# Kernel optimization log

Hardware: AMD Instinct MI355X
Metric: run time of the kernel (lower is better)

## Reference

```python
import jax, jax.numpy as jnp
import numpy as np

BS, CH, T = 128, 16, 12288
RED = 6          # mini_window_temporal_reduction_factor
N = CH * RED     # 96 mini-windows
K = 5            # top-k selected mini-windows
NCLS = 5
LATENT = (T // 16) * 8  # hypernet flatten dim = 6144


def _conv1d(x, w, b=None):
    # x: [B,C,L], w: [O,I,ks] -> [B,O,L-ks+1]
    out = jax.lax.conv_general_dilated(x, w, (1,), 'VALID', dimension_numbers=('NCH', 'OIH', 'NCH'))
    return out if b is None else out + b[None, :, None]


def _same_reflect(x, w, b):
    p = (w.shape[-1] - 1) // 2
    return _conv1d(jnp.pad(x, ((0, 0), (0, 0), (p, p)), mode='reflect'), w, b)


def _leaky(z):
    return jnp.where(z >= 0, z, 0.01 * z)


def _pool(x, f, op):
    L = x.shape[-1] // f  # floor, drop remainder (matches torch pooling)
    xr = x[..., :L * f].reshape(x.shape[:-1] + (L, f))
    return op(xr, -1)


def setup_inputs() -> dict:
    key = jax.random.key(0)
    ks = jax.random.split(key, 18)
    s = 0.05
    return {
        'x': jax.random.normal(ks[0], (BS, CH, T), jnp.float32),
        'epoch': 0,
        # hypernet conv blocks (padding='same', reflect)
        'hw1': jax.random.normal(ks[1], (32, CH, 7), jnp.float32) * s,
        'hb1': jnp.zeros((32,), jnp.float32),
        'hw2': jax.random.normal(ks[2], (64, 32, 7), jnp.float32) * s,
        'hb2': jnp.zeros((64,), jnp.float32),
        'hw3': jax.random.normal(ks[3], (8, 64, 7), jnp.float32) * s,
        'hb3': jnp.zeros((8,), jnp.float32),
        'hl1': jax.random.normal(ks[4], (N, LATENT), jnp.float32) * s,  # Linear(latent->N), no bias
        'hl2': jax.random.normal(ks[5], (N, N), jnp.float32) * s,       # Linear(N->N), no bias
        # GroupedIdxConv1D: per-group Conv1d(1, 64, ks=15); bias only for group 0
        'gw': jax.random.normal(ks[6], (CH, 64, 15), jnp.float32) * s,
        'gb0': jax.random.normal(ks[7], (64,), jnp.float32) * s,
        # encoder convs 1,2
        'ew2': jax.random.normal(ks[8], (128, 64, 7), jnp.float32) * s,
        'eb2': jnp.zeros((128,), jnp.float32),
        'ew3': jax.random.normal(ks[9], (128, 128, 7), jnp.float32) * s,
        'eb3': jnp.zeros((128,), jnp.float32),
        # classifier
        'cw': jax.random.normal(ks[10], (NCLS, 128), jnp.float32) * s,
        'cb': jnp.zeros((NCLS,), jnp.float32),
    }


def reference(x, epoch, hw1, hb1, hw2, hb2, hw3, hb3, hl1, hl2, gw, gb0, ew2, eb2, ew3, eb3, cw, cb):
    # Eval-mode forward (active sampling, no Gumbel noise, hard top-k one-hot, dropout off)
    bs = x.shape[0]
    # ---- hypernet ----
    h = _pool(_leaky(_same_reflect(x, hw1, hb1)), 4, jnp.mean)
    h = _pool(_leaky(_same_reflect(h, hw2, hb2)), 4, jnp.mean)
    h = jnp.tanh(_same_reflect(h, hw3, hb3)).reshape(bs, -1)
    logits = _leaky(h @ hl1.T) @ hl2.T  # [bs, N]
    # ---- hard top-k sampling (bmm with one-hot == gather rows) ----
    _, idx = jax.lax.top_k(logits, K)                      # [bs, K]
    x_r = x.reshape(bs, N, -1)                             # [bs, N, T']
    sel = jnp.take_along_axis(x_r, idx[:, :, None], axis=1)  # [bs, K, T']
    gidx = idx // RED                                      # ExG channel group per mini-window
    # ---- GroupedIdxConv1D: per-element kernel gather + conv + sum over K ----
    ksz = gw.shape[-1]
    Lout = sel.shape[-1] - ksz + 1
    windows = jnp.stack([sel[..., i:i + Lout] for i in range(ksz)], axis=-1)  # [bs,K,Lout,ksz]
    kernels = gw[gidx]                                     # [bs,K,64,ksz]
    z = jnp.einsum('bkls,bkos->bol', windows, kernels)     # conv + sum over channel axis K
    n0 = (gidx == 0).sum(1).astype(z.dtype)                # bias only for group 0 elements
    z = z + n0[:, None, None] * gb0[None, :, None]
    # ---- encoder tail ----
    z = _pool(_leaky(z), 4, jnp.max)
    z = _pool(_leaky(_conv1d(z, ew2, eb2)), 4, jnp.max)
    z = _conv1d(z, ew3, eb3).mean(-1)                      # AdaptiveAvgPool1d(1) -> [bs,128]
    # ---- classifier ----
    return jax.nn.log_softmax(z @ cw.T + cb, -1)           # [bs, NCLS]
```

## Files before the change

kernel.cpp:

```cpp
#include <hip/hip_runtime.h>
#include <hip/hip_bf16.h>
#include <math.h>

typedef unsigned short u16;
typedef __attribute__((ext_vector_type(8))) short short8;
typedef __attribute__((ext_vector_type(4))) float floatx4;

__device__ __forceinline__ float lk(float v){ return v >= 0.f ? v : 0.01f*v; }
__device__ __forceinline__ u16 f2b(float f){
    __hip_bfloat16 h = __float2bfloat16(f);
    return *reinterpret_cast<u16*>(&h);
}
__device__ __forceinline__ int refl(int t, int L){
    return t < 0 ? -t : (t >= L ? 2*L-2-t : t);
}

__global__ __launch_bounds__(256,6) void k_hconv1(const float* __restrict__ x,
        const float* __restrict__ w, const float* __restrict__ bias,
        u16* __restrict__ h1)
{
    __shared__ __align__(16) u16 xs[2][264*24];
    int b = blockIdx.x / 24, pb = blockIdx.x % 24;
    int tid = threadIdx.x;
    const float* xb = x + (size_t)b*16*12288;
    int wv = tid >> 6, lane = tid & 63;
    int m = lane & 15, kq = lane >> 4;
    int ohalf = wv & 1, thalf = wv >> 1;
    int o = ohalf*16 + m;

    short8 wfr[4];
    #pragma unroll
    for (int s=0;s<4;s++){
        int tap = 2*s + (kq>>1);
        #pragma unroll
        for (int j=0;j<8;j++){
            int ic = (kq&1)*8 + j;
            wfr[s][j] = (tap < 7) ? (short)f2b(w[(o*16+ic)*7 + tap]) : (short)0;
        }
    }

    float rg0[16]; float rgx;
    int exrow = 256 + (tid>>4), exch = tid & 15;

#define LOADTILE(G0) { \
        int t0 = refl((G0) - 3 + tid, 12288); \
        _Pragma("unroll") \
        for (int ic=0;ic<16;ic++) rg0[ic] = xb[(size_t)ic*12288 + t0]; \
        if (tid < 128){ \
            int t1 = refl((G0) - 3 + exrow, 12288); \
            rgx = xb[(size_t)exch*12288 + t1]; \
        } }

#define WRITETILE(BUF) { \
        short8 p0, p1; \
        _Pragma("unroll") \
        for (int j=0;j<8;j++){ p0[j] = (short)f2b(rg0[j]); p1[j] = (short)f2b(rg0[8+j]); } \
        *reinterpret_cast<short8*>(&xs[BUF][tid*24])     = p0; \
        *reinterpret_cast<short8*>(&xs[BUF][tid*24 + 8]) = p1; \
        if (tid < 128) xs[BUF][exrow*24 + exch] = f2b(rgx); }

#define COMPUTESTORE(BUF, TILE) { \
        floatx4 acc[8]; \
        _Pragma("unroll") \
        for (int i=0;i<8;i++) acc[i] = (floatx4){0.f,0.f,0.f,0.f}; \
        int tb0 = thalf*128; \
        _Pragma("unroll") \
        for (int sub=0; sub<8; sub++){ \
            int tb = tb0 + sub*16; \
            _Pragma("unroll") \
            for (int s=0;s<4;s++){ \
                int tap = 2*s + (kq>>1); \
                short8 xfr = *reinterpret_cast<const short8*>( \
                                &xs[BUF][(tb + m + tap)*24 + (kq&1)*8]); \
                acc[sub] = __builtin_amdgcn_mfma_f32_16x16x32_bf16(xfr, wfr[s], acc[sub], 0,0,0); \
            } \
        } \
        float bv = bias[o]; \
        size_t base = ((size_t)b*3072 + (TILE)*64 + thalf*32 + kq)*32 + o; \
        _Pragma("unroll") \
        for (int sub=0; sub<8; sub++){ \
            float sum = lk(acc[sub][0]+bv) + lk(acc[sub][1]+bv) \
                      + lk(acc[sub][2]+bv) + lk(acc[sub][3]+bv); \
            h1[base + (size_t)sub*128] = f2b(sum*0.25f); \
        } }

    int g0 = pb*512;
    LOADTILE(g0);
    WRITETILE(0);
    __syncthreads();
    LOADTILE(g0 + 256);
    COMPUTESTORE(0, pb*2);
    WRITETILE(1);
    __syncthreads();
    COMPUTESTORE(1, pb*2 + 1);

#undef LOADTILE
#undef WRITETILE
#undef COMPUTESTORE
}

__global__ __launch_bounds__(256,4) void k_hconv2(const u16* __restrict__ h1,
        const float* __restrict__ w, const float* __restrict__ bias,
        float* __restrict__ h2)
{
    __shared__ __align__(16) u16 xs[2][198*40];
    int b = blockIdx.x >> 3, tile = blockIdx.x & 7;
    int tid = threadIdx.x;
    int wv = tid >> 6, lane = tid & 63;
    int m = lane & 15, kq = lane >> 4;
    int o = wv*16 + m;

    short8 wfr[7];
    #pragma unroll
    for (int s=0;s<7;s++){
        #pragma unroll
        for (int j=0;j<8;j++)
            wfr[s][j] = (short)f2b(w[(size_t)(o*32 + kq*8 + j)*7 + s]);
    }

    short8 rgA[3], rgX;

#define LOADH(HALF) { \
        int gh = tile*384 + (HALF)*192 - 3; \
        _Pragma("unroll") \
        for (int cc=0;cc<3;cc++){ \
            int c = tid + cc*256; \
            int row = c >> 2, q = c & 3; \
            int t = refl(gh + row, 3072); \
            rgA[cc] = *reinterpret_cast<const short8*>(&h1[((size_t)b*3072 + t)*32 + q*8]); \
        } \
        if (tid < 24){ \
            int c = 768 + tid; \
            int row = c >> 2, q = c & 3; \
            int t = refl(gh + row, 3072); \
            rgX = *reinterpret_cast<const short8*>(&h1[((size_t)b*3072 + t)*32 + q*8]); \
        } }

#define WRITEH(BUF) { \
        _Pragma("unroll") \
        for (int cc=0;cc<3;cc++){ \
            int c = tid + cc*256; \
            *reinterpret_cast<short8*>(&xs[BUF][(c>>2)*40 + (c&3)*8]) = rgA[cc]; \
        } \
        if (tid < 24){ \
            int c = 768 + tid; \
            *reinterpret_cast<short8*>(&xs[BUF][(c>>2)*40 + (c&3)*8]) = rgX; \
        } }

#define COMPUTEH(BUF, HALF) { \
        floatx4 acc[12]; \
        _Pragma("unroll") \
        for (int i=0;i<12;i++) acc[i] = (floatx4){0.f,0.f,0.f,0.f}; \
        for (int sub=0; sub<12; sub++){ \
            int tb = sub*16; \
            _Pragma("unroll") \
            for (int s=0;s<7;s++){ \
                short8 xfr = *reinterpret_cast<const short8*>( \
                                &xs[BUF][(tb + m + s)*40 + kq*8]); \
                acc[sub] = __builtin_amdgcn_mfma_f32_16x16x32_bf16(xfr, wfr[s], acc[sub], 0,0,0); \
            } \
        } \
        float bv = bias[o]; \
        _Pragma("unroll") \
        for (int sub=0; sub<12; sub++){ \
            float sum = lk(acc[sub][0]+bv) + lk(acc[sub][1]+bv) \
                      + lk(acc[sub][2]+bv) + lk(acc[sub][3]+bv); \
            h2[((size_t)b*768 + tile*96 + (HALF)*48 + sub*4 + kq)*64 + o] = sum*0.25f; \
        } }

    LOADH(0);
    WRITEH(0);
    __syncthreads();
    LOADH(1);
    COMPUTEH(0, 0);
    WRITEH(1);
    __syncthreads();
    COMPUTEH(1, 1);

#undef LOADH
#undef WRITEH
#undef COMPUTEH
}

__global__ __launch_bounds__(256) void k_hconv3(const float* __restrict__ h2,
        const float* __restrict__ w, const float* __restrict__ bias,
        float* __restrict__ latent)
{
    __shared__ float xs[64*201];
    int b = blockIdx.x >> 2, tile = blockIdx.x & 3;
    int g0 = tile*192;
    int tid = threadIdx.x;
    for (int idx = tid; idx < 198*64; idx += 256){
        int jj = idx >> 6, ic = idx & 63;
        int t = refl(g0 + jj - 3, 768);
        xs[ic*201 + jj] = h2[((size_t)b*768 + t)*64 + ic];
    }
    __syncthreads();
    int c = tid >> 5, run = tid & 31;
    int p0 = run*6;
    float acc[6];
    #pragma unroll
    for (int l=0;l<6;l++) acc[l] = 0.f;
    for (int ic=0; ic<64; ic++){
        const float* wp = w + (c*64+ic)*7;
        float wr[7];
        #pragma unroll
        for (int s=0;s<7;s++) wr[s] = wp[s];
        const float* xr = xs + ic*201 + p0;
        float xw[12];
        #pragma unroll
        for (int j=0;j<12;j++) xw[j] = xr[j];
        #pragma unroll
        for (int s=0;s<7;s++)
            #pragma unroll
            for (int l=0;l<6;l++) acc[l] += wr[s]*xw[l+s];
    }
    float bv = bias[c];
    float* op = latent + (size_t)b*6144 + c*768 + g0 + p0;
    #pragma unroll
    for (int l=0;l<6;l++) op[l] = tanhf(acc[l] + bv);
}

__global__ __launch_bounds__(256) void k_lin1(const float* __restrict__ latent,
        const float* __restrict__ hl1, float* __restrict__ t1)
{
    __shared__ float ls[6144];
    int b = blockIdx.x / 6, ntile = blockIdx.x % 6;
    int tid = threadIdx.x;
    const float4* lp = reinterpret_cast<const float4*>(latent + (size_t)b*6144);
    float4* lsv = reinterpret_cast<float4*>(ls);
    for (int i = tid; i < 1536; i += 256) lsv[i] = lp[i];
    __syncthreads();
    int wv = tid >> 6, lane = tid & 63;
    #pragma unroll
    for (int nn=0; nn<4; nn++){
        int n = ntile*16 + wv*4 + nn;
        const float4* wp = reinterpret_cast<const float4*>(hl1 + (size_t)n*6144);
        float s = 0.f;
        #pragma unroll
        for (int j=0;j<24;j++){
            float4 q = wp[lane + 64*j];
            float4 l4 = lsv[lane + 64*j];
            s += l4.x*q.x + l4.y*q.y + l4.z*q.z + l4.w*q.w;
        }
        #pragma unroll
        for (int off=32; off; off>>=1) s += __shfl_down(s, off);
        if (lane==0) t1[b*96+n] = lk(s);
    }
}

__global__ __launch_bounds__(128) void k_topk(const float* __restrict__ t1,
        const float* __restrict__ hl2, int* __restrict__ idxb, float* __restrict__ n0f)
{
    __shared__ float lg[96];
    int b = blockIdx.x, n = threadIdx.x;
    if (n < 96){
        float s = 0.f;
        const float* tp = t1 + b*96;
        const float* wp = hl2 + n*96;
        for (int m=0;m<96;m++) s += tp[m]*wp[m];
        lg[n] = s;
    }
    __syncthreads();
    if (threadIdx.x == 0){
        unsigned long long u0=0ull, u1=0ull;
        float n0 = 0.f;
        for (int k=0;k<5;k++){
            float best = -3.4e38f; int bi = 0;
            for (int m=0;m<96;m++){
                bool used = m<64 ? ((u0>>m)&1ull) : ((u1>>(m-64))&1ull);
                if (!used && lg[m] > best){ best = lg[m]; bi = m; }
            }
            if (bi<64) u0 |= 1ull<<bi; else u1 |= 1ull<<(bi-64);
            idxb[b*5+k] = bi;
            if (bi < 6) n0 += 1.f;
        }
        n0f[b] = n0;
    }
}

__global__ __launch_bounds__(256,3) void k_gconv(const float* __restrict__ x,
        const int* __restrict__ idxb, const float* __restrict__ n0f,
        const float* __restrict__ gw, const float* __restrict__ gb0,
        u16* __restrict__ zp)
{
    __shared__ __align__(16) u16 xs[5][8][536];
    __shared__ int nidx[5];
    __shared__ float n0s;
    int b = blockIdx.x >> 2, qc = blockIdx.x & 3;
    int tid = threadIdx.x;
    int p0g = qc*512;

    if (tid < 5) nidx[tid] = idxb[b*5 + tid];
    if (tid == 5) n0s = n0f[b];
    __syncthreads();

    for (int cch = tid; cch < 5*134; cch += 256){
        int k = cch / 134, q = cch - k*134;
        const float* xrow = x + (size_t)b*196608 + (size_t)nidx[k]*2048;
        int base = p0g + q*4;
        u16 vb[4];
        if (base + 3 <= 2047){
            float4 a = *reinterpret_cast<const float4*>(xrow + base);
            vb[0]=f2b(a.x); vb[1]=f2b(a.y); vb[2]=f2b(a.z); vb[3]=f2b(a.w);
        } else {
            #pragma unroll
            for (int jj=0;jj<4;jj++){
                int ii = base+jj; if (ii > 2047) ii = 2047;
                vb[jj] = f2b(xrow[ii]);
            }
        }
        #pragma unroll
        for (int jj=0;jj<4;jj++){
            int gof = q*4 + jj;
            #pragma unroll
            for (int r=0;r<8;r++){
                int i = gof - r;
                if (i >= 0 && i < 528) xs[k][r][i] = vb[jj];
            }
        }
    }

    int wv = tid >> 6, lane = tid & 63;
    int m = lane & 15, kq = lane >> 4;
    int o = wv*16 + m;

    short8 wfr[3];
    #pragma unroll
    for (int c=0;c<3;c++){
        #pragma unroll
        for (int j=0;j<8;j++){
            int k = 32*c + kq*8 + j;
            int kk = k >> 4, tap = k & 15;
            short v = 0;
            if (kk < 5 && tap < 15){
                int gi = nidx[kk] / 6;
                v = (short)f2b(gw[(size_t)gi*960 + o*15 + tap]);
            }
            wfr[c][j] = v;
        }
    }
    float bv = n0s * gb0[o];
    __syncthreads();

    int rr = m & 7, ibase = (m & 8) + (kq & 1)*8;
    for (int g8 = 0; g8 < 4; ++g8){
        floatx4 acc[8];
        #pragma unroll
        for (int i=0;i<8;i++) acc[i] = (floatx4){0.f,0.f,0.f,0.f};
        #pragma unroll
        for (int s8=0; s8<8; ++s8){
            int P = (g8*8 + s8)*16;
            #pragma unroll
            for (int c=0;c<3;c++){
                int kk = 2*c + (kq>>1);
                int kkc = kk < 5 ? kk : 4;
                short8 af = *reinterpret_cast<const short8*>(&xs[kkc][rr][P + ibase]);
                acc[s8] = __builtin_amdgcn_mfma_f32_16x16x32_bf16(af, wfr[c], acc[s8], 0,0,0);
            }
        }
        #pragma unroll
        for (int s8=0; s8<8; ++s8){
            int sub = g8*8 + s8;
            int Q = qc*128 + sub*4 + kq;
            if (Q < 508){
                float mx = fmaxf(fmaxf(lk(acc[s8][0]+bv), lk(acc[s8][1]+bv)),
                                 fmaxf(lk(acc[s8][2]+bv), lk(acc[s8][3]+bv)));
                zp[((size_t)b*508 + Q)*64 + o] = f2b(mx);
            }
        }
    }
}

__global__ __launch_bounds__(256,1) void k_econv2(const u16* __restrict__ zp,
        const float* __restrict__ w, const float* __restrict__ bias,
        float* __restrict__ p2)
{
    __shared__ __align__(16) u16 xs[118*72];
    int b = blockIdx.x / 5, tile = blockIdx.x % 5;
    int tid = threadIdx.x;
    for (int c = tid; c < 118*8; c += 256){
        int row = c >> 3, q = c & 7;
        int t = tile*100 + row; if (t > 507) t = 507;
        *reinterpret_cast<short8*>(&xs[row*72 + q*8]) =
            *reinterpret_cast<const short8*>(&zp[((size_t)b*508 + t)*64 + q*8]);
    }
    __syncthreads();
    int wv = tid >> 6, lane = tid & 63;
    int m = lane & 15, kq = lane >> 4;
    for (int half=0; half<2; half++){
        int ot = wv + 4*half;
        int o = ot*16 + m;
        short8 wfr[14];
        #pragma unroll
        for (int s=0;s<14;s++){
            int ih = s/7, tap = s%7;
            #pragma unroll
            for (int j=0;j<8;j++)
                wfr[s][j] = (short)f2b(w[(size_t)(o*64 + ih*32 + kq*8 + j)*7 + tap]);
        }
        floatx4 acc[7];
        #pragma unroll
        for (int i=0;i<7;i++) acc[i] = (floatx4){0.f,0.f,0.f,0.f};
        #pragma unroll
        for (int sub=0; sub<7; sub++){
            #pragma unroll
            for (int s=0;s<14;s++){
                int ih = s/7, tap = s%7;
                short8 xfr = *reinterpret_cast<const short8*>(
                                &xs[(sub*16 + m + tap)*72 + ih*32 + kq*8]);
                acc[sub] = __builtin_amdgcn_mfma_f32_16x16x32_bf16(xfr, wfr[s], acc[sub], 0,0,0);
            }
        }
        float bv = bias[o];
        #pragma unroll
        for (int sub=0; sub<7; sub++){
            int pidx = sub*4 + kq;
            if (pidx < 25){
                float mx = fmaxf(fmaxf(lk(acc[sub][0]+bv), lk(acc[sub][1]+bv)),
                                 fmaxf(lk(acc[sub][2]+bv), lk(acc[sub][3]+bv)));
                p2[((size_t)b*125 + tile*25 + pidx)*128 + o] = mx;
            }
        }
    }
}

__global__ __launch_bounds__(128) void k_tail(const float* __restrict__ p2,
        const float* __restrict__ w, const float* __restrict__ bias,
        const float* __restrict__ cw, const float* __restrict__ cb,
        float* __restrict__ out)
{
    __shared__ float ss[7][128];
    __shared__ float ft[128];
    __shared__ float lgs[5];
    int b = blockIdx.x, tid = threadIdx.x;

    {
        const float* pb = p2 + (size_t)b*125*128 + tid;
        float first6[6], last6[6];
        float c = 0.f;
        #pragma unroll
        for (int t=0;t<6;t++){ float v = pb[(size_t)t*128]; first6[t]=v; c+=v; }
        for (int t=6;t<119;t++) c += pb[(size_t)t*128];
        #pragma unroll
        for (int t=0;t<6;t++) last6[t] = pb[(size_t)(119+t)*128];
        ss[0][tid] = c;
        #pragma unroll
        for (int s=0;s<6;s++){ c = c - first6[s] + last6[s]; ss[s+1][tid] = c; }
    }
    __syncthreads();

    {
        const float* wp = w + (size_t)tid*896;
        float s = 0.f;
        for (int ic=0; ic<128; ic++){
            #pragma unroll
            for (int tp=0; tp<7; tp++)
                s += wp[ic*7+tp]*ss[tp][ic];
        }
        ft[tid] = s*(1.f/119.f) + bias[tid];
    }
    __syncthreads();

    if (tid < 5){
        float lg = cb[tid];
        const float* wp = cw + tid*128;
        for (int o=0;o<128;o++) lg += ft[o]*wp[o];
        lgs[tid] = lg;
    }
    __syncthreads();
    if (tid == 0){
        float mx = -3.4e38f;
        for (int c=0;c<5;c++) mx = fmaxf(mx, lgs[c]);
        float se = 0.f;
        for (int c=0;c<5;c++) se += expf(lgs[c]-mx);
        float lse = mx + logf(se);
        for (int c=0;c<5;c++) out[b*5+c] = lgs[c]-lse;
    }
}

extern "C" void kernel_launch(void* const* d_in, const int* in_sizes, int n_in,
                              void* d_out, int out_size, void* d_ws, size_t ws_size,
                              hipStream_t stream)
{
    const float* x   = (const float*)d_in[0];
    const float* hw1 = (const float*)d_in[2];
    const float* hb1 = (const float*)d_in[3];
    const float* hw2 = (const float*)d_in[4];
    const float* hb2 = (const float*)d_in[5];
    const float* hw3 = (const float*)d_in[6];
    const float* hb3 = (const float*)d_in[7];
    const float* hl1 = (const float*)d_in[8];
    const float* hl2 = (const float*)d_in[9];
    const float* gw  = (const float*)d_in[10];
    const float* gb0 = (const float*)d_in[11];
    const float* ew2 = (const float*)d_in[12];
    const float* eb2 = (const float*)d_in[13];
    const float* ew3 = (const float*)d_in[14];
    const float* eb3 = (const float*)d_in[15];
    const float* cw  = (const float*)d_in[16];
    const float* cb  = (const float*)d_in[17];
    float* out = (float*)d_out;

    float* f       = (float*)d_ws;
    float* latent  = f;
    float* t1      = f + 786432;
    int*   idxb    = (int*)(f + 806432);
    float* n0f     = f + 808432;
    u16*   zpb     = (u16*)(f + 810000);
    float* h2      = f + 3932160;
    float* p2      = f + 5000000;
    u16*   h1b     = (u16*)(f + 10223616);

    k_hconv1<<<3072, 256, 0, stream>>>(x, hw1, hb1, h1b);
    k_hconv2<<<1024, 256, 0, stream>>>(h1b, hw2, hb2, h2);
    k_hconv3<<<512, 256, 0, stream>>>(h2, hw3, hb3, latent);
    k_lin1<<<768, 256, 0, stream>>>(latent, hl1, t1);
    k_topk<<<128, 128, 0, stream>>>(t1, hl2, idxb, n0f);
    k_gconv<<<512, 256, 0, stream>>>(x, idxb, n0f, gw, gb0, zpb);
    k_econv2<<<640, 256, 0, stream>>>(zpb, ew2, eb2, p2);
    k_tail<<<128, 128, 0, stream>>>(p2, ew3, eb3, cw, cb, out);
}
```

Baseline: 407.8 us.

## Prepack bf16 MFMA weight fragments once and stage hconv1 output through LDS

Adds a prep kernel that converts the conv weights to bf16 and lays them out in MFMA fragment order, so each block loads one short8 per fragment instead of doing eight strided fp32 loads and conversions. hconv1 now writes its pooled outputs into an LDS buffer and stores them to global as coalesced 16-byte vectors, and its occupancy hint drops from 6 to 4. Scheduling barriers are added after the tile loads. The cost is one extra kernel launch, a bit more LDS per block and one more barrier.

After: 358.9 us. 12.0% less time.

```diff
diff --git a/kernel.cpp b/kernel.cpp
--- a/kernel.cpp
+++ b/kernel.cpp
@@ -15,11 +15,35 @@
     return t < 0 ? -t : (t >= L ? 2*L-2-t : t);
 }
 
-__global__ __launch_bounds__(256,6) void k_hconv1(const float* __restrict__ x,
-        const float* __restrict__ w, const float* __restrict__ bias,
+__global__ __launch_bounds__(256) void k_prep(const float* __restrict__ hw1,
+        const float* __restrict__ hw2, const float* __restrict__ ew2,
+        const float* __restrict__ gw, u16* __restrict__ wb)
+{
+    int idx = blockIdx.x*256 + threadIdx.x;
+    if (idx < 4096){
+        int u = idx; int j=u&7; int o=(u>>3)&31; int kq=(u>>8)&3; int s=u>>10;
+        int tap = 2*s + (kq>>1); int ic = (kq&1)*8 + j;
+        wb[idx] = (tap<7) ? f2b(hw1[(o*16+ic)*7+tap]) : (u16)0;
+    } else if (idx < 18432){
+        int u = idx - 4096; int j=u&7; int o=(u>>3)&63; int kq=(u>>9)&3; int s=u>>11;
+        wb[idx] = f2b(hw2[(o*32 + kq*8 + j)*7 + s]);
+    } else if (idx < 75776){
+        int u = idx - 18432; int j=u&7; int o=(u>>3)&127; int kq=(u>>10)&3; int s=u>>12;
+        int ih = s/7, tap = s-ih*7;
+        wb[idx] = f2b(ew2[(o*64 + ih*32 + kq*8 + j)*7 + tap]);
+    } else if (idx < 92160){
+        int u = idx - 75776; int j=u&7; int o=(u>>3)&63; int tb=(u>>9)&1; int gi=u>>10;
+        int tap = tb*8 + j;
+        wb[idx] = (tap<15) ? f2b(gw[gi*960 + o*15 + tap]) : (u16)0;
+    }
+}
+
+__global__ __launch_bounds__(256,4) void k_hconv1(const float* __restrict__ x,
+        const u16* __restrict__ wb1, const float* __restrict__ bias,
         u16* __restrict__ h1)
 {
     __shared__ __align__(16) u16 xs[2][264*24];
+    __shared__ __align__(16) u16 ob[2][64*32];
     int b = blockIdx.x / 24, pb = blockIdx.x % 24;
     int tid = threadIdx.x;
     const float* xb = x + (size_t)b*16*12288;
@@ -30,14 +54,9 @@
 
     short8 wfr[4];
     #pragma unroll
-    for (int s=0;s<4;s++){
-        int tap = 2*s + (kq>>1);
-        #pragma unroll
-        for (int j=0;j<8;j++){
-            int ic = (kq&1)*8 + j;
-            wfr[s][j] = (tap < 7) ? (short)f2b(w[(o*16+ic)*7 + tap]) : (short)0;
-        }
-    }
+    for (int s=0;s<4;s++)
+        wfr[s] = *reinterpret_cast<const short8*>(&wb1[(((s*4+kq)*32)+o)*8]);
+    float bv = bias[o];
 
     float rg0[16]; float rgx;
     int exrow = 256 + (tid>>4), exch = tid & 15;
@@ -49,7 +68,8 @@
         if (tid < 128){ \
             int t1 = refl((G0) - 3 + exrow, 12288); \
             rgx = xb[(size_t)exch*12288 + t1]; \
-        } }
+        } \
+        __builtin_amdgcn_sched_barrier(0); }
 
 #define WRITETILE(BUF) { \
         short8 p0, p1; \
@@ -59,7 +79,7 @@
         *reinterpret_cast<short8*>(&xs[BUF][tid*24 + 8]) = p1; \
         if (tid < 128) xs[BUF][exrow*24 + exch] = f2b(rgx); }
 
-#define COMPUTESTORE(BUF, TILE) { \
+#define COMPUTETILE(BUF) { \
         floatx4 acc[8]; \
         _Pragma("unroll") \
         for (int i=0;i<8;i++) acc[i] = (floatx4){0.f,0.f,0.f,0.f}; \
@@ -75,32 +95,38 @@
                 acc[sub] = __builtin_amdgcn_mfma_f32_16x16x32_bf16(xfr, wfr[s], acc[sub], 0,0,0); \
             } \
         } \
-        float bv = bias[o]; \
-        size_t base = ((size_t)b*3072 + (TILE)*64 + thalf*32 + kq)*32 + o; \
         _Pragma("unroll") \
         for (int sub=0; sub<8; sub++){ \
             float sum = lk(acc[sub][0]+bv) + lk(acc[sub][1]+bv) \
                       + lk(acc[sub][2]+bv) + lk(acc[sub][3]+bv); \
-            h1[base + (size_t)sub*128] = f2b(sum*0.25f); \
+            ob[BUF][(thalf*32 + sub*4 + kq)*32 + o] = f2b(sum*0.25f); \
         } }
+
+#define STORETILE(BUF, TILE) { \
+        short8 v = *reinterpret_cast<const short8*>(&ob[BUF][tid*8]); \
+        *reinterpret_cast<short8*>(&h1[((size_t)b*3072 + (TILE)*64)*32 + tid*8]) = v; }
 
     int g0 = pb*512;
     LOADTILE(g0);
     WRITETILE(0);
     __syncthreads();
     LOADTILE(g0 + 256);
-    COMPUTESTORE(0, pb*2);
+    COMPUTETILE(0);
     WRITETILE(1);
     __syncthreads();
-    COMPUTESTORE(1, pb*2 + 1);
+    STORETILE(0, pb*2);
+    COMPUTETILE(1);
+    __syncthreads();
+    STORETILE(1, pb*2 + 1);
 
 #undef LOADTILE
 #undef WRITETILE
-#undef COMPUTESTORE
+#undef COMPUTETILE
+#undef STORETILE
 }
 
 __global__ __launch_bounds__(256,4) void k_hconv2(const u16* __restrict__ h1,
-        const float* __restrict__ w, const float* __restrict__ bias,
+        const u16* __restrict__ wb2, const float* __restrict__ bias,
         float* __restrict__ h2)
 {
     __shared__ __align__(16) u16 xs[2][198*40];
@@ -112,11 +138,9 @@
 
     short8 wfr[7];
     #pragma unroll
-    for (int s=0;s<7;s++){
-        #pragma unroll
-        for (int j=0;j<8;j++)
-            wfr[s][j] = (short)f2b(w[(size_t)(o*32 + kq*8 + j)*7 + s]);
-    }
+    for (int s=0;s<7;s++)
+        wfr[s] = *reinterpret_cast<const short8*>(&wb2[(((s*4+kq)*64)+o)*8]);
+    float bv = bias[o];
 
     short8 rgA[3], rgX;
 
@@ -134,7 +158,8 @@
             int row = c >> 2, q = c & 3; \
             int t = refl(gh + row, 3072); \
             rgX = *reinterpret_cast<const short8*>(&h1[((size_t)b*3072 + t)*32 + q*8]); \
-        } }
+        } \
+        __builtin_amdgcn_sched_barrier(0); }
 
 #define WRITEH(BUF) { \
         _Pragma("unroll") \
@@ -160,7 +185,6 @@
                 acc[sub] = __builtin_amdgcn_mfma_f32_16x16x32_bf16(xfr, wfr[s], acc[sub], 0,0,0); \
             } \
         } \
-        float bv = bias[o]; \
         _Pragma("unroll") \
         for (int sub=0; sub<12; sub++){ \
             float sum = lk(acc[sub][0]+bv) + lk(acc[sub][1]+bv) \
@@ -281,7 +305,7 @@
 
 __global__ __launch_bounds__(256,3) void k_gconv(const float* __restrict__ x,
         const int* __restrict__ idxb, const float* __restrict__ n0f,
-        const float* __restrict__ gw, const float* __restrict__ gb0,
+        const u16* __restrict__ gwb, const float* __restrict__ gb0,
         u16* __restrict__ zp)
 {
     __shared__ __align__(16) u16 xs[5][8][536];
@@ -328,17 +352,13 @@
     short8 wfr[3];
     #pragma unroll
     for (int c=0;c<3;c++){
-        #pragma unroll
-        for (int j=0;j<8;j++){
-            int k = 32*c + kq*8 + j;
-            int kk = k >> 4, tap = k & 15;
-            short v = 0;
-            if (kk < 5 && tap < 15){
-                int gi = nidx[kk] / 6;
-                v = (short)f2b(gw[(size_t)gi*960 + o*15 + tap]);
-            }
-            wfr[c][j] = v;
-        }
+        int kk = 2*c + (kq>>1);
+        int kkc = kk < 5 ? kk : 4;
+        int gi = nidx[kkc] / 6;
+        short8 f = *reinterpret_cast<const short8*>(
+                        &gwb[(((gi*2 + (kq&1))*64)+o)*8]);
+        if (kk >= 5) f = (short8)(short)0;
+        wfr[c] = f;
     }
     float bv = n0s * gb0[o];
     __syncthreads();
@@ -373,7 +393,7 @@
 }
 
 __global__ __launch_bounds__(256,1) void k_econv2(const u16* __restrict__ zp,
-        const float* __restrict__ w, const float* __restrict__ bias,
+        const u16* __restrict__ wbe, const float* __restrict__ bias,
         float* __restrict__ p2)
 {
     __shared__ __align__(16) u16 xs[118*72];
@@ -393,12 +413,8 @@
         int o = ot*16 + m;
         short8 wfr[14];
         #pragma unroll
-        for (int s=0;s<14;s++){
-            int ih = s/7, tap = s%7;
-            #pragma unroll
-            for (int j=0;j<8;j++)
-                wfr[s][j] = (short)f2b(w[(size_t)(o*64 + ih*32 + kq*8 + j)*7 + tap]);
-        }
+        for (int s=0;s<14;s++)
+            wfr[s] = *reinterpret_cast<const short8*>(&wbe[(((s*4+kq)*128)+o)*8]);
         floatx4 acc[7];
         #pragma unroll
         for (int i=0;i<7;i++) acc[i] = (floatx4){0.f,0.f,0.f,0.f};
@@ -406,7 +422,7 @@
         for (int sub=0; sub<7; sub++){
             #pragma unroll
             for (int s=0;s<14;s++){
-                int ih = s/7, tap = s%7;
+                int tap = s%7, ih = s/7;
                 short8 xfr = *reinterpret_cast<const short8*>(
                                 &xs[(sub*16 + m + tap)*72 + ih*32 + kq*8]);
                 acc[sub] = __builtin_amdgcn_mfma_f32_16x16x32_bf16(xfr, wfr[s], acc[sub], 0,0,0);
@@ -508,16 +524,18 @@
     int*   idxb    = (int*)(f + 806432);
     float* n0f     = f + 808432;
     u16*   zpb     = (u16*)(f + 810000);
+    u16*   wb      = (u16*)(f + 2900000);
     float* h2      = f + 3932160;
     float* p2      = f + 5000000;
     u16*   h1b     = (u16*)(f + 10223616);
 
-    k_hconv1<<<3072, 256, 0, stream>>>(x, hw1, hb1, h1b);
-    k_hconv2<<<1024, 256, 0, stream>>>(h1b, hw2, hb2, h2);
+    k_prep<<<360, 256, 0, stream>>>(hw1, hw2, ew2, gw, wb);
+    k_hconv1<<<3072, 256, 0, stream>>>(x, wb, hb1, h1b);
+    k_hconv2<<<1024, 256, 0, stream>>>(h1b, wb + 4096, hb2, h2);
     k_hconv3<<<512, 256, 0, stream>>>(h2, hw3, hb3, latent);
     k_lin1<<<768, 256, 0, stream>>>(latent, hl1, t1);
     k_topk<<<128, 128, 0, stream>>>(t1, hl2, idxb, n0f);
-    k_gconv<<<512, 256, 0, stream>>>(x, idxb, n0f, gw, gb0, zpb);
-    k_econv2<<<640, 256, 0, stream>>>(zpb, ew2, eb2, p2);
+    k_gconv<<<512, 256, 0, stream>>>(x, idxb, n0f, wb + 75776, gb0, zpb);
+    k_econv2<<<640, 256, 0, stream>>>(zpb, wb + 18432, eb2, p2);
     k_tail<<<128, 128, 0, stream>>>(p2, ew3, eb3, cw, cb, out);
 }
```
